# Kernel optimization log

Measured on AMD Instinct MI355X. Metric: run time of the kernel, lower is better.

## Reference

```python
import jax, jax.numpy as jnp
import numpy as np

B, S, D, H = 2, 2048, 2048, 16
HD = D // H  # 128


def setup_inputs() -> dict:
    key = jax.random.key(0)
    ks = jax.random.split(key, 6)
    sc = 0.02
    return {
        "x": jax.random.normal(ks[0], (B, S, D), jnp.float32),
        "attention_mask": jnp.ones((B, S), jnp.int32),
        "w_qkv": jax.random.normal(ks[1], (D, 3 * D), jnp.float32) * sc,
        "b_qkv": jnp.zeros((3 * D,), jnp.float32),
        "w_o": jax.random.normal(ks[2], (D, D), jnp.float32) * sc,
        "b_o": jnp.zeros((D,), jnp.float32),
        "ln1_w": jnp.ones((D,), jnp.float32),
        "w1": jax.random.normal(ks[3], (D, 8 * D), jnp.float32) * sc,
        "b1": jnp.zeros((8 * D,), jnp.float32),
        "w2": jax.random.normal(ks[4], (4 * D, D), jnp.float32) * sc,
        "b2": jnp.zeros((D,), jnp.float32),
        "ln2_w": jnp.ones((D,), jnp.float32),
    }


def rmsnorm(x, w, eps=1e-6):
    rms = jnp.sqrt(jnp.mean(x * x, axis=-1, keepdims=True) + eps)
    return w * (x / rms)


def rope_tables(seq_len, dim, base=10000.0):
    inv_freq = 1.0 / (base ** (jnp.arange(0, dim, 2, dtype=jnp.float32) / dim))
    t = jnp.arange(seq_len, dtype=jnp.float32)
    freqs = t[:, None] * inv_freq[None, :]          # [S, dim/2]
    emb = jnp.concatenate([freqs, freqs], axis=-1)  # [S, dim]
    return jnp.cos(emb), jnp.sin(emb)


def apply_rope(x, cos, sin):
    # Faithful to source: rotate pairs, then out = rot*cos + roll(rot,1)*sin
    xr = x.reshape(*x.shape[:-1], -1, 2)
    x1, x2 = xr[..., 0], xr[..., 1]
    rot = jnp.stack([-x2, x1], axis=-1).reshape(x.shape)
    return rot * cos + jnp.roll(rot, shift=1, axis=-1) * sin


def transformer_layer(x, attention_mask, w_qkv, b_qkv, w_o, b_o, ln1_w, w1, b1, w2, b2, ln2_w):
    residual = x
    qkv = x @ w_qkv + b_qkv                         # [B,S,3D]
    q, k, v = jnp.split(qkv, 3, axis=-1)
    split = lambda t: t.reshape(B, S, H, HD).transpose(0, 2, 1, 3)  # [B,H,S,HD]
    q, k, v = split(q), split(k), split(v)

    cos, sin = rope_tables(S, HD)                   # [S,HD], broadcasts over B,H
    q = apply_rope(q, cos, sin)
    k = apply_rope(k, cos, sin)

    scores = jnp.einsum("bhqd,bhkd->bhqk", q, k) / jnp.sqrt(jnp.float32(HD))
    mask = (attention_mask == 1)[:, None, None, :]  # [B,1,1,S]
    scores = jnp.where(mask, scores, -jnp.inf)
    attn = jax.nn.softmax(scores, axis=-1)
    out = jnp.einsum("bhqk,bhkd->bhqd", attn, v)
    out = out.transpose(0, 2, 1, 3).reshape(B, S, D)
    out = out @ w_o + b_o

    x = rmsnorm(out + residual, ln1_w)
    residual = x
    h = x @ w1 + b1                                 # [B,S,8D]
    h, gate = jnp.split(h, 2, axis=-1)
    h = h * jax.nn.gelu(gate, approximate=False)
    h = h @ w2 + b2
    return rmsnorm(h + residual, ln2_w)


def reference(x, attention_mask, w_qkv, b_qkv, w_o, b_o, ln1_w, w1, b1, w2, b2, ln2_w):
    return transformer_layer(x, attention_mask, w_qkv, b_qkv, w_o, b_o, ln1_w, w1, b1, w2, b2, ln2_w)
```

## Files before the change

### kernel.cpp

```cpp
#include <hip/hip_runtime.h>
#include <cstdint>
#include <cstring>

typedef unsigned short u16;
typedef __attribute__((ext_vector_type(8))) short short8;
typedef __attribute__((ext_vector_type(8))) unsigned short ushortx8;
typedef __attribute__((ext_vector_type(4))) float floatx4;

#define DEV __device__ __forceinline__

DEV u16 f2bf(float f) {
  union { float f; uint32_t u; } x; x.f = f;
  uint32_t r = x.u + 0x7fffu + ((x.u >> 16) & 1u);
  return (u16)(r >> 16);
}
DEV float bf2f(u16 h) {
  union { float f; uint32_t u; } x; x.u = ((uint32_t)h) << 16;
  return x.f;
}
DEV u16 f2h(float f) {
  union { u16 u; _Float16 h; } x; x.h = (_Float16)f; return x.u;
}
DEV float h2f(u16 h) {
  union { u16 u; _Float16 h; } x; x.u = h; return (float)x.h;
}
DEV float fexp2(float x) { return __builtin_amdgcn_exp2f(x); }
DEV float fast_gelu(float g) {
  float u = 0.7978845608f * (g + 0.044715f * g * g * g);
  float e = fexp2(-2.885390082f * fabsf(u));
  float th = (1.0f - e) / (1.0f + e);
  th = (u < 0.0f) ? -th : th;
  return 0.5f * g * (1.0f + th);
}
DEV void gload_lds16(const void* g, void* lds) {
  __builtin_amdgcn_global_load_lds(
      (const __attribute__((address_space(1))) char*)(uintptr_t)g,
      (__attribute__((address_space(3))) char*)(uintptr_t)lds, 16, 0, 0);
}

__global__ __launch_bounds__(256) void k_prep(const float* __restrict__ x,
                                              u16* __restrict__ xb,
                                              const float* __restrict__ Wq,
                                              u16* __restrict__ WqT,
                                              const float* __restrict__ Wo,
                                              u16* __restrict__ WoT,
                                              const float* __restrict__ W2,
                                              u16* __restrict__ W2T,
                                              const float* __restrict__ W1,
                                              u16* __restrict__ W1Tp,
                                              float* __restrict__ ct,
                                              float* __restrict__ st) {
  __shared__ u16 t[64][70];
  const int id = blockIdx.x;
  if (id < 4096) {
    int i = (id * 256 + (int)threadIdx.x) * 8;
    float4 a = *(const float4*)(x + i);
    float4 b = *(const float4*)(x + i + 4);
    ushortx8 o;
    o[0] = f2bf(a.x); o[1] = f2bf(a.y); o[2] = f2bf(a.z); o[3] = f2bf(a.w);
    o[4] = f2bf(b.x); o[5] = f2bf(b.y); o[6] = f2bf(b.z); o[7] = f2bf(b.w);
    *(ushortx8*)(xb + i) = o;
  } else if (id < 20480) {
    const float* W; u16* Wt; int R, C, c0, r0;
    int src;
    int cx = threadIdx.x & 15, ry = threadIdx.x >> 4;
    if (id < 12288) {
      int tix;
      int i2 = id - 4096;
      if (i2 < 3072)      { W = Wq; Wt = WqT; R = 2048; C = 6144; tix = i2; }
      else if (i2 < 4096) { W = Wo; Wt = WoT; R = 2048; C = 2048; tix = i2 - 3072; }
      else                { W = W2; Wt = W2T; R = 8192; C = 2048; tix = i2 - 4096; }
      int ntc = C >> 6;
      c0 = (tix % ntc) * 64; r0 = (tix / ntc) * 64;
      src = c0 + cx * 4;
    } else {
      int iw = id - 12288;
      W = W1; Wt = W1Tp; R = 2048; C = 16384;
      c0 = (iw & 255) * 64; r0 = (iw >> 8) * 64;
      int eta = c0 + cx * 4;
      int Bq = eta >> 8, ii = eta & 255, wn = (ii >> 6) & 3, rr = ii & 63,
          n = rr >> 4, tt = rr & 15;
      src = Bq * 128 + wn * 32 + (n & 1) * 16 + tt + ((n >= 2) ? 8192 : 0);
    }
#pragma unroll
    for (int i = 0; i < 4; ++i) {
      int row = ry + i * 16;
      float4 v = *(const float4*)(W + (size_t)(r0 + row) * C + src);
      ushort2 lo, hi;
      lo.x = f2bf(v.x); lo.y = f2bf(v.y);
      hi.x = f2bf(v.z); hi.y = f2bf(v.w);
      *(ushort2*)&t[row][cx * 4] = lo;
      *(ushort2*)&t[row][cx * 4 + 2] = hi;
    }
    __syncthreads();
#pragma unroll
    for (int i = 0; i < 4; ++i) {
      int col = ry + i * 16;
      ushort4 o;
      o.x = t[cx * 4 + 0][col]; o.y = t[cx * 4 + 1][col];
      o.z = t[cx * 4 + 2][col]; o.w = t[cx * 4 + 3][col];
      *(ushort4*)(Wt + (size_t)(c0 + col) * R + r0 + cx * 4) = o;
    }
  } else {
    int i = (id - 20480) * 256 + (int)threadIdx.x;
    int s = i >> 6, j = i & 63;
    float invf = 1.0f / powf(10000.0f, (float)j * (1.0f / 64.0f));
    float ang = (float)s * invf;
    ct[i] = cosf(ang);
    st[i] = sinf(ang);
  }
}

__global__ __launch_bounds__(512, 1) void k_gemm128(const u16* __restrict__ A,
                                                    const u16* __restrict__ Bt,
                                                    const float* __restrict__ bias,
                                                    u16* __restrict__ qrO,
                                                    u16* __restrict__ krO,
                                                    u16* __restrict__ vtO,
                                                    const float* __restrict__ ctabO,
                                                    const float* __restrict__ stabO) {
  constexpr int K = 2048;
  constexpr int nt = K / 32;
  __shared__ __align__(16) u16 lds[4][12288];
  const int tid = threadIdx.x;
  const int w = tid >> 6, lane = tid & 63;
  const int l15 = lane & 15, l4 = lane >> 4;
  const int wm = w >> 2, wn = w & 3;
  const int xcd = blockIdx.x & 7, loc = blockIdx.x >> 3;
  const int swz = xcd * 96 + loc;
  const int bm = swz / 24, bn = swz % 24;

  const size_t abase = (size_t)bm * 128 * K;
  const size_t bbase = (size_t)bn * 256 * K;

  const int srA = tid >> 2;
  const int scA = (tid & 3) ^ ((srA >> 1) & 3);
  auto stageA = [&](int kt) {
    gload_lds16(A + abase + (size_t)srA * K + kt * 32 + scA * 8,
                (void*)&lds[kt & 3][(size_t)tid * 8]);
  };
  auto stageB = [&](int kt, int li) {
    int g = li * 512 + tid;
    int row = g >> 2;
    int sc = (g & 3) ^ ((row >> 1) & 3);
    gload_lds16(Bt + bbase + (size_t)row * K + kt * 32 + sc * 8,
                (void*)&lds[kt & 3][4096 + (size_t)g * 8]);
  };
  const int fro = l15 * 32 + (l4 ^ ((l15 >> 1) & 3)) * 8;

  floatx4 acc[4][4];
  floatx4 zero = {0.f, 0.f, 0.f, 0.f};
#pragma unroll
  for (int m = 0; m < 4; ++m)
#pragma unroll
    for (int n = 0; n < 4; ++n) acc[m][n] = zero;

  for (int kt = 0; kt < 3; ++kt) { stageA(kt); stageB(kt, 0); stageB(kt, 1); }

  for (int t = 0; t < nt; ++t) {
    const int buf = t & 3;
    if (t < nt - 2)       asm volatile("s_waitcnt vmcnt(6)" ::: "memory");
    else if (t == nt - 2) asm volatile("s_waitcnt vmcnt(3)" ::: "memory");
    else                  asm volatile("s_waitcnt vmcnt(0)" ::: "memory");
    __builtin_amdgcn_sched_barrier(0);
    __builtin_amdgcn_s_barrier();
    const u16* Ab = &lds[buf][wm * 2048 + fro];
    const u16* Bb = &lds[buf][4096 + wn * 2048 + fro];
    short8 av[4], bv[4];
#pragma unroll
    for (int n = 0; n < 4; ++n) bv[n] = *(const short8*)(Bb + n * 512);
    av[0] = *(const short8*)(Ab);
    av[1] = *(const short8*)(Ab + 512);
    if (t + 3 < nt) { stageA(t + 3); stageB(t + 3, 0); }
    asm volatile("s_waitcnt lgkmcnt(0)" ::: "memory");
    __builtin_amdgcn_sched_barrier(0);
    __builtin_amdgcn_s_setprio(1);
#pragma unroll
    for (int i = 0; i < 2; ++i)
#pragma unroll
      for (int n = 0; n < 4; ++n)
        acc[i][n] = __builtin_amdgcn_mfma_f32_16x16x32_bf16(av[i], bv[n], acc[i][n], 0, 0, 0);
    __builtin_amdgcn_s_setprio(0);
    __builtin_amdgcn_s_barrier();
    av[2] = *(const short8*)(Ab + 2 * 512);
    av[3] = *(const short8*)(Ab + 3 * 512);
    if (t + 3 < nt) stageB(t + 3, 1);
    asm volatile("s_waitcnt lgkmcnt(0)" ::: "memory");
    __builtin_amdgcn_sched_barrier(0);
    __builtin_amdgcn_s_setprio(1);
#pragma unroll
    for (int i = 0; i < 2; ++i)
#pragma unroll
      for (int n = 0; n < 4; ++n)
        acc[2 + i][n] = __builtin_amdgcn_mfma_f32_16x16x32_bf16(av[2 + i], bv[n], acc[2 + i][n], 0, 0, 0);
    __builtin_amdgcn_s_setprio(0);
  }

  constexpr int PAD = 264;
  u16* T = (u16*)lds;
  __syncthreads();
#pragma unroll
  for (int n = 0; n < 4; ++n) {
    float bb = bias[bn * 256 + wn * 64 + n * 16 + l15];
#pragma unroll
    for (int m = 0; m < 4; ++m)
#pragma unroll
      for (int j = 0; j < 4; ++j)
        T[(wm * 64 + m * 16 + l4 * 4 + j) * PAD + wn * 64 + n * 16 + l15] =
            f2bf(acc[m][n][j] + bb);
  }
  __syncthreads();
  const int bq = bm >> 4;
  const int srow0 = (bm & 15) * 128;
  if (bn < 16) {
    int sl = tid >> 2, hh = (tid >> 1) & 1, t2 = tid & 1;
    const u16* row = T + sl * PAD + hh * 128;
    int s = srow0 + sl;
    int head = 2 * (bn & 7) + hh;
    u16* dst = (bn < 8 ? qrO : krO) +
               (((size_t)bq * 16 + head) * 2048 + s) * 128 + t2 * 64;
    const float* ctr = ctabO + (s << 6);
    const float* str2 = stabO + (s << 6);
    const float qs = (bn < 8) ? 0.12751744f : 1.0f;
#pragma unroll
    for (int ch = 0; ch < 8; ++ch) {
      int d0 = t2 * 64 + ch * 8;
      ushortx8 xv = *(const ushortx8*)(row + d0);
      float xp = bf2f(row[(d0 + 126) & 127]);
      int f0 = d0 & 63;
      float4 c0v = *(const float4*)(ctr + f0);
      float4 c1v = *(const float4*)(ctr + f0 + 4);
      float4 s0v = *(const float4*)(str2 + f0);
      float4 s1v = *(const float4*)(str2 + f0 + 4);
      float cc[8] = {c0v.x, c0v.y, c0v.z, c0v.w, c1v.x, c1v.y, c1v.z, c1v.w};
      float sn[8] = {s0v.x, s0v.y, s0v.z, s0v.w, s1v.x, s1v.y, s1v.z, s1v.w};
      ushortx8 o;
#pragma unroll
      for (int pr = 0; pr < 4; ++pr) {
        float xe = bf2f((u16)xv[2 * pr]), xo = bf2f((u16)xv[2 * pr + 1]);
        o[2 * pr]     = f2bf((-xo * cc[2 * pr] + xp * sn[2 * pr]) * qs);
        o[2 * pr + 1] = f2bf(( xe * cc[2 * pr + 1] - xo * sn[2 * pr + 1]) * qs);
        xp = xe;
      }
      *(ushortx8*)(dst + ch * 8) = o;
    }
  } else {
    int hh = tid >> 8, dg = (tid >> 4) & 15, sc2 = tid & 15;
    int head = 2 * (bn - 16) + hh;
    int s0 = srow0 + sc2 * 8;
    ushortx8 r[8];
#pragma unroll
    for (int i = 0; i < 8; ++i)
      r[i] = *(const ushortx8*)(T + (sc2 * 8 + i) * PAD + hh * 128 + dg * 8);
    u16* vbase = vtO + ((size_t)bq * 2048 + head * 128 + dg * 8) * 2048 + s0;
#pragma unroll
    for (int j2 = 0; j2 < 8; ++j2) {
      ushortx8 o;
#pragma unroll
      for (int i = 0; i < 8; ++i) o[i] = r[i][j2];
      *(ushortx8*)(vbase + (size_t)j2 * 2048) = o;
    }
  }
}

template <int EPI>
__global__ __launch_bounds__(512, 2) void k_gemm256(const u16* __restrict__ A,
                                                    const u16* __restrict__ Bt,
                                                    void* __restrict__ C,
                                                    const float* __restrict__ bias,
                                                    int M, int N, int K, int nsplit) {
  __shared__ __align__(16) u16 lds[4][2][8192];
  const int tid = threadIdx.x;
  const int w = tid >> 6, lane = tid & 63;
  const int l15 = lane & 15, l4 = lane >> 4;
  const int wm = w >> 2, wn = w & 3;
  const int nbn = N >> 8;
  const int nbm = M >> 8;

  int bm, bn, split = 0;
  if (nsplit == 1 && nbm == 16 && (nbn & 7) == 0) {
    const int xcd = blockIdx.x & 7, l = blockIdx.x >> 3;
    const int xr = xcd >> 1, xc = xcd & 1;
    const int stn = l >> 4, lbm = (l >> 2) & 3, lbn = l & 3;
    bm = xr * 4 + lbm;
    bn = xc * (nbn >> 1) + stn * 4 + lbn;
  } else {
    const int nwg = gridDim.x;
    const int q = nwg >> 3, r8 = nwg & 7;
    const int xcd = blockIdx.x & 7, loc = blockIdx.x >> 3;
    const int swz = (xcd < r8 ? xcd * (q + 1) : r8 * (q + 1) + (xcd - r8) * q) + loc;
    const int ntiles = nwg / nsplit;
    split = swz / ntiles;
    const int tix = swz % ntiles;
    bm = tix / nbn; bn = tix % nbn;
  }
  const int klen = K / nsplit;
  const int kofs = split * klen;

  const size_t abase = (size_t)bm * 256 * K + kofs;
  const size_t bbase = (size_t)bn * 256 * K + kofs;
  const int nt = klen >> 5;

  const int sr = tid >> 2;
  const int sc = (tid & 3) ^ ((sr >> 1) & 3);
  auto stage = [&](int kt, int li, int op) {
    const u16* src = op ? (Bt + bbase) : (A + abase);
    gload_lds16(src + (size_t)(li * 128 + sr) * K + kt * 32 + sc * 8,
                (void*)&lds[kt & 3][op][(li * 512 + w * 64) * 8]);
  };

  const int fro = l15 * 32 + (l4 ^ ((l15 >> 1) & 3)) * 8;

  floatx4 acc[8][4];
  floatx4 zero = {0.f, 0.f, 0.f, 0.f};
#pragma unroll
  for (int m = 0; m < 8; ++m)
#pragma unroll
    for (int n = 0; n < 4; ++n) acc[m][n] = zero;

  for (int kt = 0; kt < 3; ++kt)
    if (kt < nt) {
      stage(kt, 0, 0); stage(kt, 0, 1);
      stage(kt, 1, 0); stage(kt, 1, 1);
    }

  for (int t = 0; t < nt; ++t) {
    const int buf = t & 3;
    if (t < nt - 2)       asm volatile("s_waitcnt vmcnt(8)" ::: "memory");
    else if (t == nt - 2) asm volatile("s_waitcnt vmcnt(4)" ::: "memory");
    else                  asm volatile("s_waitcnt vmcnt(0)" ::: "memory");
    __builtin_amdgcn_sched_barrier(0);
    __builtin_amdgcn_s_barrier();
    const u16* Ab = &lds[buf][0][wm * 4096 + fro];
    const u16* Bb = &lds[buf][1][wn * 2048 + fro];
    short8 av[4], bv[4];
#pragma unroll
    for (int n = 0; n < 4; ++n) bv[n] = *(const short8*)(Bb + n * 512);
#pragma unroll
    for (int i = 0; i < 4; ++i) av[i] = *(const short8*)(Ab + i * 512);
    if (t + 3 < nt) { stage(t + 3, 0, 0); stage(t + 3, 0, 1); }
    asm volatile("s_waitcnt lgkmcnt(0)" ::: "memory");
    __builtin_amdgcn_sched_barrier(0);
    __builtin_amdgcn_s_setprio(1);
#pragma unroll
    for (int i = 0; i < 4; ++i)
#pragma unroll
      for (int n = 0; n < 4; ++n)
        acc[i][n] = __builtin_amdgcn_mfma_f32_16x16x32_bf16(av[i], bv[n], acc[i][n], 0, 0, 0);
    __builtin_amdgcn_s_setprio(0);
    __builtin_amdgcn_s_barrier();
#pragma unroll
    for (int i = 0; i < 4; ++i) av[i] = *(const short8*)(Ab + (4 + i) * 512);
    if (t + 3 < nt) { stage(t + 3, 1, 0); stage(t + 3, 1, 1); }
    asm volatile("s_waitcnt lgkmcnt(0)" ::: "memory");
    __builtin_amdgcn_sched_barrier(0);
    __builtin_amdgcn_s_setprio(1);
#pragma unroll
    for (int i = 0; i < 4; ++i)
#pragma unroll
      for (int n = 0; n < 4; ++n)
        acc[4 + i][n] = __builtin_amdgcn_mfma_f32_16x16x32_bf16(av[i], bv[n], acc[4 + i][n], 0, 0, 0);
    __builtin_amdgcn_s_setprio(0);
  }

  const int row0 = bm * 256 + wm * 128, col0 = bn * 256 + wn * 64;
  if (EPI == 2) {
    u16* P = (u16*)C + (size_t)split * M * N;
#pragma unroll
    for (int n = 0; n < 4; ++n) {
      int col = col0 + n * 16 + l15;
#pragma unroll
      for (int m = 0; m < 8; ++m)
#pragma unroll
        for (int j = 0; j < 4; ++j) {
          int row = row0 + m * 16 + l4 * 4 + j;
          P[(size_t)row * N + col] = f2h(acc[m][n][j]);
        }
    }
  } else if (EPI == 3) {
    __syncthreads();
    u16* ep = ((u16*)lds) + w * 4096;
    const int colA = bn * 128 + wn * 32;
#pragma unroll
    for (int n = 0; n < 2; ++n) {
      float ba = bias[colA + n * 16 + l15];
      float bg = bias[8192 + colA + n * 16 + l15];
#pragma unroll
      for (int m = 0; m < 8; ++m)
#pragma unroll
        for (int j = 0; j < 4; ++j) {
          float a = acc[m][n][j] + ba;
          float g = acc[m][n + 2][j] + bg;
          ep[(m * 16 + l4 * 4 + j) * 32 + n * 16 + l15] = f2bf(a * fast_gelu(g));
        }
    }
    const int rr = lane >> 2, cg = lane & 3;
    u16* Cg = (u16*)C;
    const int Nact = N >> 1;
#pragma unroll
    for (int pass = 0; pass < 8; ++pass) {
      short8 v = *(const short8*)&ep[(pass * 16 + rr) * 32 + cg * 8];
      size_t grow = row0 + pass * 16 + rr;
      *(short8*)&Cg[grow * Nact + colA + cg * 8] = v;
    }
  } else {
    __syncthreads();
    u16* ep = ((u16*)lds) + w * 8192;
#pragma unroll
    for (int n = 0; n < 4; ++n) {
      float bb = bias[col0 + n * 16 + l15];
#pragma unroll
      for (int m = 0; m < 8; ++m)
#pragma unroll
        for (int j = 0; j < 4; ++j)
          ep[(m * 16 + l4 * 4 + j) * 64 + n * 16 + l15] = f2bf(acc[m][n][j] + bb);
    }
    const int rr = lane >> 3, cg = lane & 7;
    u16* Cg = (u16*)C;
#pragma unroll
    for (int pass = 0; pass < 16; ++pass) {
      short8 v = *(const short8*)&ep[(pass * 8 + rr) * 64 + cg * 8];
      size_t grow = row0 + pass * 8 + rr;
      *(short8*)&Cg[grow * N + col0 + cg * 8] = v;
    }
  }
}

__global__ __launch_bounds__(512, 4) void k_attn(const u16* __restrict__ Qr,
                                                 const u16* __restrict__ Kr,
                                                 const u16* __restrict__ Vt,
                                                 const int* __restrict__ mask,
                                                 u16* __restrict__ O) {
  constexpr int S = 2048, HD = 128, H = 16;
  __shared__ __align__(16) u16 Ksh[64 * 128];
  __shared__ __align__(16) u16 Vsh[128 * 64];
  __shared__ __align__(16) u16 Psh[8][16 * 72];
  __shared__ float Msh[2048];

  const int bid = blockIdx.x;
  const int xcd = bid & 7, local = bid >> 3;
  const int bh = xcd * 4 + (local >> 4);
  const int qt = local & 15;
  const int b = bh >> 4, h = bh & 15;
  const int tid = threadIdx.x, wave = tid >> 6, lane = tid & 63;
  const int l15 = lane & 15, l4 = lane >> 4;
  const size_t bhs = (size_t)(b * H + h);
  const u16* Qb = Qr + bhs * S * HD;
  const u16* Kb = Kr + bhs * S * HD;
  const u16* Vb = Vt + bhs * HD * S;

  for (int i = tid; i < 2048; i += 512)
    Msh[i] = (mask[b * S + i] == 1) ? 0.0f : -1e30f;

  const int qrow = qt * 128 + wave * 16 + l15;
  short8 qf[4];
#pragma unroll
  for (int kk = 0; kk < 4; ++kk)
    qf[kk] = *(const short8*)&Qb[(size_t)qrow * HD + kk * 32 + l4 * 8];

  const int giA = tid, giB = 512 + tid;
  const int rKA = giA >> 4, gKA = giA & 15;
  const int rKB = giB >> 4, gKB = giB & 15;
  const int gsKA = (gKA & 8) | ((gKA ^ rKA) & 7);
  const int gsKB = (gKB & 8) | ((gKB ^ rKB) & 7);
  const int rVA = giA >> 3, gVA = giA & 7;
  const int rVB = giB >> 3, gVB = giB & 7;
  const int gsVA = (gVA ^ rVA) & 7;
  const int gsVB = (gVB ^ rVB) & 7;
  const u16* pKA = Kb + (size_t)rKA * HD + gsKA * 8;
  const u16* pKB = Kb + (size_t)rKB * HD + gsKB * 8;
  const u16* pVA = Vb + (size_t)rVA * S + gsVA * 8;
  const u16* pVB = Vb + (size_t)rVB * S + gsVB * 8;

  float m_run[4], l_run[4];
  floatx4 o_acc[8];
  floatx4 zero = {0.f, 0.f, 0.f, 0.f};
#pragma unroll
  for (int j = 0; j < 4; ++j) { m_run[j] = -1e30f; l_run[j] = 0.f; }
#pragma unroll
  for (int n = 0; n < 8; ++n) o_acc[n] = zero;

  uint4 k0 = *(const uint4*)pKA;
  uint4 k1 = *(const uint4*)pKB;
  uint4 v0 = *(const uint4*)pVA;
  uint4 v1 = *(const uint4*)pVB;

  for (int ktile = 0; ktile < S / 64; ++ktile) {
    __builtin_amdgcn_sched_barrier(0);
    __builtin_amdgcn_s_barrier();
    __builtin_amdgcn_sched_barrier(0);
    *(uint4*)&Ksh[(size_t)(0 * 512 + tid) * 8] = k0;
    *(uint4*)&Ksh[(size_t)(1 * 512 + tid) * 8] = k1;
    *(uint4*)&Vsh[(size_t)(0 * 512 + tid) * 8] = v0;
    *(uint4*)&Vsh[(size_t)(1 * 512 + tid) * 8] = v1;
    if (ktile + 1 < S / 64) {
      k0 = *(const uint4*)(pKA + (size_t)(ktile + 1) * 8192);
      k1 = *(const uint4*)(pKB + (size_t)(ktile + 1) * 8192);
      v0 = *(const uint4*)(pVA + (size_t)(ktile + 1) * 64);
      v1 = *(const uint4*)(pVB + (size_t)(ktile + 1) * 64);
    }
    asm volatile("s_waitcnt lgkmcnt(0)" ::: "memory");
    __builtin_amdgcn_sched_barrier(0);
    __builtin_amdgcn_s_barrier();
    __builtin_amdgcn_sched_barrier(0);

    floatx4 s_acc[4];
#pragma unroll
    for (int nf = 0; nf < 4; ++nf) s_acc[nf] = zero;
    __builtin_amdgcn_s_setprio(1);
#pragma unroll
    for (int kk = 0; kk < 4; ++kk) {
#pragma unroll
      for (int nf = 0; nf < 4; ++nf) {
        int key = nf * 16 + l15;
        int G = kk * 4 + l4;
        int lg = (G & 8) | ((G ^ key) & 7);
        short8 kv = *(const short8*)&Ksh[key * 128 + lg * 8];
        s_acc[nf] = __builtin_amdgcn_mfma_f32_16x16x32_bf16(qf[kk], kv, s_acc[nf], 0, 0, 0);
      }
    }
    __builtin_amdgcn_s_setprio(0);

    float p[4][4];
#pragma unroll
    for (int nf = 0; nf < 4; ++nf) {
      float ma = Msh[ktile * 64 + nf * 16 + l15];
#pragma unroll
      for (int j = 0; j < 4; ++j) p[nf][j] = s_acc[nf][j] + ma;
    }
#pragma unroll
    for (int j = 0; j < 4; ++j) {
      float mx = fmaxf(fmaxf(p[0][j], p[1][j]), fmaxf(p[2][j], p[3][j]));
      mx = fmaxf(mx, __shfl_xor(mx, 1));
      mx = fmaxf(mx, __shfl_xor(mx, 2));
      mx = fmaxf(mx, __shfl_xor(mx, 4));
      mx = fmaxf(mx, __shfl_xor(mx, 8));
      float mnew = fmaxf(m_run[j], mx);
      float corr = fexp2(m_run[j] - mnew);
      float ps = 0.f;
#pragma unroll
      for (int nf = 0; nf < 4; ++nf) {
        p[nf][j] = fexp2(p[nf][j] - mnew);
        ps += p[nf][j];
      }
      l_run[j] = l_run[j] * corr + ps;
      m_run[j] = mnew;
#pragma unroll
      for (int n = 0; n < 8; ++n) o_acc[n][j] *= corr;
    }

#pragma unroll
    for (int nf = 0; nf < 4; ++nf)
#pragma unroll
      for (int j = 0; j < 4; ++j)
        Psh[wave][(l4 * 4 + j) * 72 + nf * 16 + l15] = f2bf(p[nf][j]);

    __builtin_amdgcn_s_setprio(1);
#pragma unroll
    for (int ks = 0; ks < 2; ++ks) {
      short8 pa = *(const short8*)&Psh[wave][l15 * 72 + ks * 32 + l4 * 8];
#pragma unroll
      for (int nf2 = 0; nf2 < 8; ++nf2) {
        int hd = nf2 * 16 + l15;
        int G = ks * 4 + l4;
        short8 vv = *(const short8*)&Vsh[hd * 64 + ((G ^ hd) & 7) * 8];
        o_acc[nf2] = __builtin_amdgcn_mfma_f32_16x16x32_bf16(pa, vv, o_acc[nf2], 0, 0, 0);
      }
    }
    __builtin_amdgcn_s_setprio(0);
  }

#pragma unroll
  for (int j = 0; j < 4; ++j) {
    float ls = l_run[j];
    ls += __shfl_xor(ls, 1); ls += __shfl_xor(ls, 2);
    ls += __shfl_xor(ls, 4); ls += __shfl_xor(ls, 8);
    l_run[j] = ls;
  }

#pragma unroll
  for (int j = 0; j < 4; ++j) {
    float inv = 1.0f / l_run[j];
    int srow = qt * 128 + wave * 16 + l4 * 4 + j;
    size_t orow = ((size_t)b * S + srow) * 2048 + h * 128;
#pragma unroll
    for (int nf2 = 0; nf2 < 8; ++nf2)
      O[orow + nf2 * 16 + l15] = f2bf(o_acc[nf2][j] * inv);
  }
}

__global__ __launch_bounds__(256) void k_rms_fuse1(const u16* __restrict__ p0,
                                                   const u16* __restrict__ p1,
                                                   const float* __restrict__ bias,
                                                   const float* __restrict__ resid,
                                                   const float* __restrict__ w,
                                                   u16* __restrict__ ob) {
  int row = blockIdx.x;
  int t = threadIdx.x;
  size_t base = (size_t)row * 2048 + t * 8;
  ushortx8 a = *(const ushortx8*)(p0 + base);
  ushortx8 b = *(const ushortx8*)(p1 + base);
  float4 r0 = *(const float4*)(resid + base);
  float4 r1 = *(const float4*)(resid + base + 4);
  float4 c0 = *(const float4*)(bias + t * 8);
  float4 c1 = *(const float4*)(bias + t * 8 + 4);
  float rr[8] = {r0.x, r0.y, r0.z, r0.w, r1.x, r1.y, r1.z, r1.w};
  float cc[8] = {c0.x, c0.y, c0.z, c0.w, c1.x, c1.y, c1.z, c1.w};
  float v[8];
#pragma unroll
  for (int e = 0; e < 8; ++e)
    v[e] = h2f((u16)a[e]) + h2f((u16)b[e]) + rr[e] + cc[e];
  float ss = 0.f;
#pragma unroll
  for (int e = 0; e < 8; ++e) ss += v[e] * v[e];
#pragma unroll
  for (int d = 1; d < 64; d <<= 1) ss += __shfl_xor(ss, d);
  __shared__ float sred[4];
  if ((t & 63) == 0) sred[t >> 6] = ss;
  __syncthreads();
  float tot = sred[0] + sred[1] + sred[2] + sred[3];
  float scale = rsqrtf(tot * (1.0f / 2048.0f) + 1e-6f);
  const float* wp = w + t * 8;
  ushort4 q0, q1;
  q0.x = f2bf(v[0] * wp[0] * scale); q0.y = f2bf(v[1] * wp[1] * scale);
  q0.z = f2bf(v[2] * wp[2] * scale); q0.w = f2bf(v[3] * wp[3] * scale);
  q1.x = f2bf(v[4] * wp[4] * scale); q1.y = f2bf(v[5] * wp[5] * scale);
  q1.z = f2bf(v[6] * wp[6] * scale); q1.w = f2bf(v[7] * wp[7] * scale);
  *(ushort4*)(ob + base) = q0;
  *(ushort4*)(ob + base + 4) = q1;
}

__global__ __launch_bounds__(256) void k_rms_fuse2(const u16* __restrict__ p0,
                                                   const u16* __restrict__ p1,
                                                   const float* __restrict__ bias,
                                                   const u16* __restrict__ residb,
                                                   const float* __restrict__ w,
                                                   float* __restrict__ of) {
  int row = blockIdx.x;
  int t = threadIdx.x;
  size_t base = (size_t)row * 2048 + t * 8;
  ushortx8 a = *(const ushortx8*)(p0 + base);
  ushortx8 b = *(const ushortx8*)(p1 + base);
  ushortx8 rb = *(const ushortx8*)(residb + base);
  float4 c0 = *(const float4*)(bias + t * 8);
  float4 c1 = *(const float4*)(bias + t * 8 + 4);
  float cc[8] = {c0.x, c0.y, c0.z, c0.w, c1.x, c1.y, c1.z, c1.w};
  float v[8];
#pragma unroll
  for (int e = 0; e < 8; ++e)
    v[e] = h2f((u16)a[e]) + h2f((u16)b[e]) + bf2f((u16)rb[e]) + cc[e];
  float ss = 0.f;
#pragma unroll
  for (int e = 0; e < 8; ++e) ss += v[e] * v[e];
#pragma unroll
  for (int d = 1; d < 64; d <<= 1) ss += __shfl_xor(ss, d);
  __shared__ float sred[4];
  if ((t & 63) == 0) sred[t >> 6] = ss;
  __syncthreads();
  float tot = sred[0] + sred[1] + sred[2] + sred[3];
  float scale = rsqrtf(tot * (1.0f / 2048.0f) + 1e-6f);
  const float* wp = w + t * 8;
  float4 f0, f1;
  f0.x = v[0] * wp[0] * scale; f0.y = v[1] * wp[1] * scale;
  f0.z = v[2] * wp[2] * scale; f0.w = v[3] * wp[3] * scale;
  f1.x = v[4] * wp[4] * scale; f1.y = v[5] * wp[5] * scale;
  f1.z = v[6] * wp[6] * scale; f1.w = v[7] * wp[7] * scale;
  *(float4*)(of + base) = f0;
  *(float4*)(of + base + 4) = f1;
}

extern "C" void kernel_launch(void* const* d_in, const int* in_sizes, int n_in,
                              void* d_out, int out_size, void* d_ws, size_t ws_size,
                              hipStream_t stream) {
  const float* x     = (const float*)d_in[0];
  const int*   amask = (const int*)d_in[1];
  const float* w_qkv = (const float*)d_in[2];
  const float* b_qkv = (const float*)d_in[3];
  const float* w_o   = (const float*)d_in[4];
  const float* b_o   = (const float*)d_in[5];
  const float* ln1_w = (const float*)d_in[6];
  const float* w1    = (const float*)d_in[7];
  const float* b1    = (const float*)d_in[8];
  const float* w2    = (const float*)d_in[9];
  const float* b2    = (const float*)d_in[10];
  const float* ln2_w = (const float*)d_in[11];
  float* out = (float*)d_out;

  char* ws = (char*)d_ws;
  u16*   xb    = (u16*)(ws + 0);
  u16*   wqkvT = (u16*)(ws + 16777216);
  u16*   woT   = (u16*)(ws + 41943040);
  u16*   w1Tp  = (u16*)(ws + 50331648);
  u16*   w2T   = (u16*)(ws + 117440512);
  float* ctab  = (float*)(ws + 150994944);
  float* stab  = (float*)(ws + 151519232);
  u16*   qr    = (u16*)(ws + 202375168);
  u16*   kr    = (u16*)(ws + 219152384);
  u16*   vt    = (u16*)(ws + 235929600);
  u16*   aout  = (u16*)(ws + 252706816);
  u16*   x1b   = (u16*)(ws + 303038464);
  u16*   p01a  = (u16*)(ws + 152043520);
  u16*   act   = (u16*)(ws + 152043520);
  u16*   p01b  = (u16*)(ws + 219152384);

  k_prep<<<20992, 256, 0, stream>>>(x, xb, w_qkv, wqkvT, w_o, woT, w2, w2T,
                                    w1, w1Tp, ctab, stab);

  k_gemm128<<<768, 512, 0, stream>>>(xb, wqkvT, b_qkv, qr, kr, vt, ctab, stab);
  k_attn<<<512, 512, 0, stream>>>(qr, kr, vt, amask, aout);

  k_gemm256<2><<<16 * 8 * 2, 512, 0, stream>>>(aout, woT, p01a, nullptr,
                                               4096, 2048, 2048, 2);
  k_rms_fuse1<<<4096, 256, 0, stream>>>(p01a, p01a + (size_t)4096 * 2048, b_o, x, ln1_w, x1b);

  k_gemm256<3><<<16 * 64, 512, 0, stream>>>(x1b, w1Tp, act, b1,
                                            4096, 16384, 2048, 1);

  k_gemm256<2><<<16 * 8 * 2, 512, 0, stream>>>(act, w2T, p01b, nullptr,
                                               4096, 2048, 8192, 2);
  k_rms_fuse2<<<4096, 256, 0, stream>>>(p01b, p01b + (size_t)4096 * 2048, b2, x1b, ln2_w, out);
}
```

Measured before the change: 811.1 us.

## Process two query tiles per attention block to reuse staged K/V tiles

The attention kernel now handles 256 query rows per block, as two groups of 128, and sweeps both groups over each K/V tile loaded into shared memory. This halves the number of blocks and the global-to-LDS traffic for K and V. In exchange, register use roughly doubles for the accumulators and Q fragments, so launch bounds drop to one block per CU. Only 256 blocks run, so occupancy and latency hiding may suffer.

```diff
diff --git a/kernel.cpp b/kernel.cpp
--- a/kernel.cpp
+++ b/kernel.cpp
@@ -426,7 +426,7 @@
   }
 }
 
-__global__ __launch_bounds__(512, 4) void k_attn(const u16* __restrict__ Qr,
+__global__ __launch_bounds__(512, 1) void k_attn(const u16* __restrict__ Qr,
                                                  const u16* __restrict__ Kr,
                                                  const u16* __restrict__ Vt,
                                                  const int* __restrict__ mask,
@@ -434,13 +434,13 @@
   constexpr int S = 2048, HD = 128, H = 16;
   __shared__ __align__(16) u16 Ksh[64 * 128];
   __shared__ __align__(16) u16 Vsh[128 * 64];
-  __shared__ __align__(16) u16 Psh[8][16 * 72];
+  __shared__ __align__(16) u16 Psh[8][2][16 * 72];
   __shared__ float Msh[2048];
 
   const int bid = blockIdx.x;
   const int xcd = bid & 7, local = bid >> 3;
-  const int bh = xcd * 4 + (local >> 4);
-  const int qt = local & 15;
+  const int bh = xcd * 4 + (local >> 3);
+  const int qt = local & 7;
   const int b = bh >> 4, h = bh & 15;
   const int tid = threadIdx.x, wave = tid >> 6, lane = tid & 63;
   const int l15 = lane & 15, l4 = lane >> 4;
@@ -452,11 +452,14 @@
   for (int i = tid; i < 2048; i += 512)
     Msh[i] = (mask[b * S + i] == 1) ? 0.0f : -1e30f;
 
-  const int qrow = qt * 128 + wave * 16 + l15;
-  short8 qf[4];
-#pragma unroll
-  for (int kk = 0; kk < 4; ++kk)
-    qf[kk] = *(const short8*)&Qb[(size_t)qrow * HD + kk * 32 + l4 * 8];
+  short8 qf[2][4];
+#pragma unroll
+  for (int g = 0; g < 2; ++g) {
+    int qrow = qt * 256 + g * 128 + wave * 16 + l15;
+#pragma unroll
+    for (int kk = 0; kk < 4; ++kk)
+      qf[g][kk] = *(const short8*)&Qb[(size_t)qrow * HD + kk * 32 + l4 * 8];
+  }
 
   const int giA = tid, giB = 512 + tid;
   const int rKA = giA >> 4, gKA = giA & 15;
@@ -472,13 +475,16 @@
   const u16* pVA = Vb + (size_t)rVA * S + gsVA * 8;
   const u16* pVB = Vb + (size_t)rVB * S + gsVB * 8;
 
-  float m_run[4], l_run[4];
-  floatx4 o_acc[8];
+  float m_run[2][4], l_run[2][4];
+  floatx4 o_acc[2][8];
   floatx4 zero = {0.f, 0.f, 0.f, 0.f};
 #pragma unroll
-  for (int j = 0; j < 4; ++j) { m_run[j] = -1e30f; l_run[j] = 0.f; }
-#pragma unroll
-  for (int n = 0; n < 8; ++n) o_acc[n] = zero;
+  for (int g = 0; g < 2; ++g) {
+#pragma unroll
+    for (int j = 0; j < 4; ++j) { m_run[g][j] = -1e30f; l_run[g][j] = 0.f; }
+#pragma unroll
+    for (int n = 0; n < 8; ++n) o_acc[g][n] = zero;
+  }
 
   uint4 k0 = *(const uint4*)pKA;
   uint4 k1 = *(const uint4*)pKB;
@@ -504,88 +510,93 @@
     __builtin_amdgcn_s_barrier();
     __builtin_amdgcn_sched_barrier(0);
 
-    floatx4 s_acc[4];
-#pragma unroll
-    for (int nf = 0; nf < 4; ++nf) s_acc[nf] = zero;
-    __builtin_amdgcn_s_setprio(1);
-#pragma unroll
-    for (int kk = 0; kk < 4; ++kk) {
+#pragma unroll
+    for (int g = 0; g < 2; ++g) {
+      floatx4 s_acc[4];
+#pragma unroll
+      for (int nf = 0; nf < 4; ++nf) s_acc[nf] = zero;
+      __builtin_amdgcn_s_setprio(1);
+#pragma unroll
+      for (int kk = 0; kk < 4; ++kk) {
+#pragma unroll
+        for (int nf = 0; nf < 4; ++nf) {
+          int key = nf * 16 + l15;
+          int G = kk * 4 + l4;
+          int lg = (G & 8) | ((G ^ key) & 7);
+          short8 kv = *(const short8*)&Ksh[key * 128 + lg * 8];
+          s_acc[nf] = __builtin_amdgcn_mfma_f32_16x16x32_bf16(qf[g][kk], kv, s_acc[nf], 0, 0, 0);
+        }
+      }
+      __builtin_amdgcn_s_setprio(0);
+
+      float p[4][4];
 #pragma unroll
       for (int nf = 0; nf < 4; ++nf) {
-        int key = nf * 16 + l15;
-        int G = kk * 4 + l4;
-        int lg = (G & 8) | ((G ^ key) & 7);
-        short8 kv = *(const short8*)&Ksh[key * 128 + lg * 8];
-        s_acc[nf] = __builtin_amdgcn_mfma_f32_16x16x32_bf16(qf[kk], kv, s_acc[nf], 0, 0, 0);
+        float ma = Msh[ktile * 64 + nf * 16 + l15];
+#pragma unroll
+        for (int j = 0; j < 4; ++j) p[nf][j] = s_acc[nf][j] + ma;
       }
-    }
-    __builtin_amdgcn_s_setprio(0);
-
-    float p[4][4];
-#pragma unroll
-    for (int nf = 0; nf < 4; ++nf) {
-      float ma = Msh[ktile * 64 + nf * 16 + l15];
-#pragma unroll
-      for (int j = 0; j < 4; ++j) p[nf][j] = s_acc[nf][j] + ma;
-    }
+#pragma unroll
+      for (int j = 0; j < 4; ++j) {
+        float mx = fmaxf(fmaxf(p[0][j], p[1][j]), fmaxf(p[2][j], p[3][j]));
+        mx = fmaxf(mx, __shfl_xor(mx, 1));
+        mx = fmaxf(mx, __shfl_xor(mx, 2));
+        mx = fmaxf(mx, __shfl_xor(mx, 4));
+        mx = fmaxf(mx, __shfl_xor(mx, 8));
+        float mnew = fmaxf(m_run[g][j], mx);
+        float corr = fexp2(m_run[g][j] - mnew);
+        float ps = 0.f;
+#pragma unroll
+        for (int nf = 0; nf < 4; ++nf) {
+          p[nf][j] = fexp2(p[nf][j] - mnew);
+          ps += p[nf][j];
+        }
+        l_run[g][j] = l_run[g][j] * corr + ps;
+        m_run[g][j] = mnew;
+#pragma unroll
+        for (int n = 0; n < 8; ++n) o_acc[g][n][j] *= corr;
+      }
+
+#pragma unroll
+      for (int nf = 0; nf < 4; ++nf)
+#pragma unroll
+        for (int j = 0; j < 4; ++j)
+          Psh[wave][g][(l4 * 4 + j) * 72 + nf * 16 + l15] = f2bf(p[nf][j]);
+
+      __builtin_amdgcn_s_setprio(1);
+#pragma unroll
+      for (int ks = 0; ks < 2; ++ks) {
+        short8 pa = *(const short8*)&Psh[wave][g][l15 * 72 + ks * 32 + l4 * 8];
+#pragma unroll
+        for (int nf2 = 0; nf2 < 8; ++nf2) {
+          int hd = nf2 * 16 + l15;
+          int G = ks * 4 + l4;
+          short8 vv = *(const short8*)&Vsh[hd * 64 + ((G ^ hd) & 7) * 8];
+          o_acc[g][nf2] = __builtin_amdgcn_mfma_f32_16x16x32_bf16(pa, vv, o_acc[g][nf2], 0, 0, 0);
+        }
+      }
+      __builtin_amdgcn_s_setprio(0);
+    }
+  }
+
+#pragma unroll
+  for (int g = 0; g < 2; ++g) {
 #pragma unroll
     for (int j = 0; j < 4; ++j) {
-      float mx = fmaxf(fmaxf(p[0][j], p[1][j]), fmaxf(p[2][j], p[3][j]));
-      mx = fmaxf(mx, __shfl_xor(mx, 1));
-      mx = fmaxf(mx, __shfl_xor(mx, 2));
-      mx = fmaxf(mx, __shfl_xor(mx, 4));
-      mx = fmaxf(mx, __shfl_xor(mx, 8));
-      float mnew = fmaxf(m_run[j], mx);
-      float corr = fexp2(m_run[j] - mnew);
-      float ps = 0.f;
-#pragma unroll
-      for (int nf = 0; nf < 4; ++nf) {
-        p[nf][j] = fexp2(p[nf][j] - mnew);
-        ps += p[nf][j];
-      }
-      l_run[j] = l_run[j] * corr + ps;
-      m_run[j] = mnew;
-#pragma unroll
-      for (int n = 0; n < 8; ++n) o_acc[n][j] *= corr;
-    }
-
-#pragma unroll
-    for (int nf = 0; nf < 4; ++nf)
-#pragma unroll
-      for (int j = 0; j < 4; ++j)
-        Psh[wave][(l4 * 4 + j) * 72 + nf * 16 + l15] = f2bf(p[nf][j]);
-
-    __builtin_amdgcn_s_setprio(1);
-#pragma unroll
-    for (int ks = 0; ks < 2; ++ks) {
-      short8 pa = *(const short8*)&Psh[wave][l15 * 72 + ks * 32 + l4 * 8];
-#pragma unroll
-      for (int nf2 = 0; nf2 < 8; ++nf2) {
-        int hd = nf2 * 16 + l15;
-        int G = ks * 4 + l4;
-        short8 vv = *(const short8*)&Vsh[hd * 64 + ((G ^ hd) & 7) * 8];
-        o_acc[nf2] = __builtin_amdgcn_mfma_f32_16x16x32_bf16(pa, vv, o_acc[nf2], 0, 0, 0);
-      }
-    }
-    __builtin_amdgcn_s_setprio(0);
-  }
-
-#pragma unroll
-  for (int j = 0; j < 4; ++j) {
-    float ls = l_run[j];
-    ls += __shfl_xor(ls, 1); ls += __shfl_xor(ls, 2);
-    ls += __shfl_xor(ls, 4); ls += __shfl_xor(ls, 8);
-    l_run[j] = ls;
-  }
-
-#pragma unroll
-  for (int j = 0; j < 4; ++j) {
-    float inv = 1.0f / l_run[j];
-    int srow = qt * 128 + wave * 16 + l4 * 4 + j;
-    size_t orow = ((size_t)b * S + srow) * 2048 + h * 128;
-#pragma unroll
-    for (int nf2 = 0; nf2 < 8; ++nf2)
-      O[orow + nf2 * 16 + l15] = f2bf(o_acc[nf2][j] * inv);
+      float ls = l_run[g][j];
+      ls += __shfl_xor(ls, 1); ls += __shfl_xor(ls, 2);
+      ls += __shfl_xor(ls, 4); ls += __shfl_xor(ls, 8);
+      l_run[g][j] = ls;
+    }
+#pragma unroll
+    for (int j = 0; j < 4; ++j) {
+      float inv = 1.0f / l_run[g][j];
+      int srow = qt * 256 + g * 128 + wave * 16 + l4 * 4 + j;
+      size_t orow = ((size_t)b * S + srow) * 2048 + h * 128;
+#pragma unroll
+      for (int nf2 = 0; nf2 < 8; ++nf2)
+        O[orow + nf2 * 16 + l15] = f2bf(o_acc[g][nf2][j] * inv);
+    }
   }
 }
 
@@ -707,7 +718,7 @@
                                     w1, w1Tp, ctab, stab);
 
   k_gemm128<<<768, 512, 0, stream>>>(xb, wqkvT, b_qkv, qr, kr, vt, ctab, stab);
-  k_attn<<<512, 512, 0, stream>>>(qr, kr, vt, amask, aout);
+  k_attn<<<256, 512, 0, stream>>>(qr, kr, vt, amask, aout);
 
   k_gemm256<2><<<16 * 8 * 2, 512, 0, stream>>>(aout, woT, p01a, nullptr,
                                                4096, 2048, 2048, 2);
```

Measured after the change: 817.8 us. Within noise of the previous version (+0.8%).
